# Optimization experiments

Measured on AMD Instinct MI355X. Metric: run time of the kernel, lower is better.

The kernel has to match this reference:

```python
import jax, jax.numpy as jnp
import numpy as np

DIM = 64
HEADS = 2
HD = DIM // HEADS          # 32
ALPHA = 4.0
KS = 5                     # dwc kernel size
MLP_H = 4 * DIM            # 256
LN_EPS = 1e-5


def layernorm(x, g, b):
    mu = jnp.mean(x, axis=-1, keepdims=True)
    var = jnp.mean(jnp.square(x - mu), axis=-1, keepdims=True)
    return (x - mu) * jax.lax.rsqrt(var + LN_EPS) * g + b


def safe_pow(x, p):
    # relu(x) ** p with well-defined value (and grad) at x <= 0
    xr = jnp.maximum(x, 0.0)
    safe = jnp.where(xr > 0, xr, 1.0)
    return jnp.where(xr > 0, safe ** p, 0.0)


def block_forward(x, H, W, ln1_g, ln1_b, w_qg, w_kv, pos_enc, scale_p, power_p,
                  dwc_w, dwc_b, w_proj, b_proj, ln2_g, ln2_b, w_fc1, b_fc1, w_fc2, b_fc2):
    B, N, C = x.shape
    h1 = layernorm(x, ln1_g, ln1_b)

    qg = h1 @ w_qg                         # [B,N,2C]
    q, gate = qg[..., :C], qg[..., C:]
    kv = h1 @ w_kv                         # [B,N,2C] (sr_ratio==1)
    k, v = kv[..., :C], kv[..., C:]
    k = k + pos_enc                        # [1,N,C]

    scale = jax.nn.softplus(scale_p)       # [1,1,C]
    power = 1.0 + ALPHA * jax.nn.sigmoid(power_p)  # [1,h,1,hd]
    q = q / scale
    k = k / scale

    # [B, h, N, hd]
    q = q.reshape(B, N, HEADS, HD).transpose(0, 2, 1, 3)
    k = k.reshape(B, N, HEADS, HD).transpose(0, 2, 1, 3)
    v = v.reshape(B, N, HEADS, HD).transpose(0, 2, 1, 3)

    q_pos = safe_pow(q, power)
    q_neg = safe_pow(-q, power)
    k_pos = safe_pow(k, power)
    k_neg = safe_pow(-k, power)

    q_sim = jnp.concatenate([q_pos, q_neg], axis=-1)   # [B,h,N,2hd]
    q_opp = jnp.concatenate([q_neg, q_pos], axis=-1)
    k_cat = jnp.concatenate([k_pos, k_neg], axis=-1)

    v1, v2 = v[..., :HD // 2], v[..., HD // 2:]

    n = N  # n_reduced == N for sr_ratio==1
    inv_sqrt_n = jnp.float32(n) ** -0.5
    k_mean = jnp.mean(k_cat, axis=-2)                  # [B,h,2hd]

    z_sim = 1.0 / (jnp.einsum('bhnd,bhd->bhn', q_sim, k_mean)[..., None] + 1e-6)
    kv_sim = jnp.einsum('bhnd,bhne->bhde', k_cat * inv_sqrt_n, v1 * inv_sqrt_n)
    x_sim = jnp.einsum('bhnd,bhde->bhne', q_sim, kv_sim) * z_sim

    z_opp = 1.0 / (jnp.einsum('bhnd,bhd->bhn', q_opp, k_mean)[..., None] + 1e-6)
    kv_opp = jnp.einsum('bhnd,bhne->bhde', k_cat * inv_sqrt_n, v2 * inv_sqrt_n)
    x_opp = jnp.einsum('bhnd,bhde->bhne', q_opp, kv_opp) * z_opp

    xa = jnp.concatenate([x_sim, x_opp], axis=-1)      # [B,h,N,hd]
    xa = xa.transpose(0, 2, 1, 3).reshape(B, N, C)

    # depthwise 5x5 conv over v in image layout
    v_img = v.reshape(B * HEADS, n, HD).transpose(0, 2, 1).reshape(B * HEADS, HD, H, W)
    v_dwc = jax.lax.conv_general_dilated(
        v_img, dwc_w, window_strides=(1, 1), padding='SAME',
        feature_group_count=HD, dimension_numbers=('NCHW', 'OIHW', 'NCHW'))
    v_dwc = v_dwc + dwc_b[None, :, None, None]
    v_dwc = v_dwc.reshape(B, C, H * W).transpose(0, 2, 1)  # [B,N,C]

    xa = (xa + v_dwc) * gate
    xa = xa @ w_proj + b_proj

    x = x + xa
    h2 = layernorm(x, ln2_g, ln2_b)
    m = jax.nn.gelu(h2 @ w_fc1 + b_fc1, approximate=False) @ w_fc2 + b_fc2
    return x + m


def setup_inputs() -> dict:
    key = jax.random.key(0)
    ks = jax.random.split(key, 12)
    B, H, W = 16, 128, 128
    N = H * W
    s = 0.02
    return {
        'x': jax.random.normal(ks[0], (B, N, DIM), jnp.float32),
        'H': H, 'W': W,
        'ln1_g': jnp.ones((DIM,), jnp.float32),
        'ln1_b': jnp.zeros((DIM,), jnp.float32),
        'w_qg': jax.random.normal(ks[1], (DIM, 2 * DIM), jnp.float32) * s,
        'w_kv': jax.random.normal(ks[2], (DIM, 2 * DIM), jnp.float32) * s,
        'pos_enc': jax.random.normal(ks[3], (1, N, DIM), jnp.float32) * s,
        'scale_p': jax.random.normal(ks[4], (1, 1, DIM), jnp.float32) * s,
        'power_p': jax.random.normal(ks[5], (1, HEADS, 1, HD), jnp.float32) * s,
        'dwc_w': jax.random.normal(ks[6], (HD, 1, KS, KS), jnp.float32) * s,
        'dwc_b': jnp.zeros((HD,), jnp.float32),
        'w_proj': jax.random.normal(ks[7], (DIM, DIM), jnp.float32) * s,
        'b_proj': jnp.zeros((DIM,), jnp.float32),
        'ln2_g': jnp.ones((DIM,), jnp.float32),
        'ln2_b': jnp.zeros((DIM,), jnp.float32),
        'w_fc1': jax.random.normal(ks[8], (DIM, MLP_H), jnp.float32) * s,
        'b_fc1': jnp.zeros((MLP_H,), jnp.float32),
        'w_fc2': jax.random.normal(ks[9], (MLP_H, DIM), jnp.float32) * s,
        'b_fc2': jnp.zeros((DIM,), jnp.float32),
    }


def reference(x, H, W, ln1_g, ln1_b, w_qg, w_kv, pos_enc, scale_p, power_p,
              dwc_w, dwc_b, w_proj, b_proj, ln2_g, ln2_b, w_fc1, b_fc1, w_fc2, b_fc2):
    return block_forward(x, H, W, ln1_g, ln1_b, w_qg, w_kv, pos_enc, scale_p, power_p,
                         dwc_w, dwc_b, w_proj, b_proj, ln2_g, ln2_b, w_fc1, b_fc1, w_fc2, b_fc2)
```

## Files before the change

kernel.cpp:

```cpp
#include <hip/hip_runtime.h>
#include <hip/hip_bf16.h>

#define NB 16
#define NT 16384
#define NTOK (NB * NT)

typedef __hip_bfloat16 bf16;
typedef __attribute__((ext_vector_type(8))) short short8;
typedef __attribute__((ext_vector_type(4))) float f32x4;

static __device__ __forceinline__ f32x4 MFMA(short8 a, short8 b, f32x4 c) {
    return __builtin_amdgcn_mfma_f32_16x16x32_bf16(a, b, c, 0, 0, 0);
}
static __device__ __forceinline__ short bfs(float f) {
    union { bf16 h; short s; } u; u.h = __float2bfloat16(f); return u.s;
}
static __device__ __forceinline__ float sbf(short s) {
    union { bf16 h; short s; } u; u.s = s; return __bfloat162float(u.h);
}
static __device__ __forceinline__ bf16 f2bf(float v) { return __float2bfloat16(v); }
static __device__ __forceinline__ float us2f(unsigned short u) {
    union { unsigned int i; float f; } x; x.i = ((unsigned int)u) << 16; return x.f;
}
static __device__ __forceinline__ unsigned char e8(float v) {
    union { _Float16 h; unsigned short u; } x; x.h = (_Float16)v;
    return (unsigned char)((x.u + 0x80) >> 8);
}
static __device__ __forceinline__ float d8(unsigned char e) {
    union { _Float16 h; unsigned short u; } x; x.u = (unsigned short)(e << 8);
    return (float)x.h;
}

static __device__ __forceinline__ float safe_pow(float x, float p) {
    return (x > 0.f) ? __builtin_amdgcn_exp2f(p * __builtin_amdgcn_logf(x)) : 0.f;
}
static __device__ __forceinline__ float sigm(float y) {
    return __builtin_amdgcn_rcpf(1.f + __builtin_amdgcn_exp2f(-1.44269504f * y));
}

static __device__ __forceinline__ int swb(int row, int tok) {
    return row * 64 + ((tok * 2) ^ (((row >> 1) & 3) << 4));
}

__global__ __launch_bounds__(256)
void k0_prep(const float* __restrict__ w_qg, const float* __restrict__ w_kv,
             const float* __restrict__ w_fc1, const float* __restrict__ w_fc2,
             short* __restrict__ wqk_f, short* __restrict__ wf1_f, short* __restrict__ wf2_f)
{
    int idx = blockIdx.x * 256 + threadIdx.x;
    if (idx < 16384) {
        int k = idx >> 8, col = idx & 255;
        float wv = (col < 128) ? w_qg[k * 128 + col] : w_kv[k * 128 + col - 128];
        int ct = col >> 4, ks = k >> 5, lane = (col & 15) + 16 * ((k & 31) >> 3), j = k & 7;
        wqk_f[((ct * 2 + ks) * 64 + lane) * 8 + j] = bfs(wv);
    } else if (idx < 32768) {
        int i2 = idx - 16384, k = i2 >> 8, col = i2 & 255;
        int ct = col >> 4, ks = k >> 5, lane = (col & 15) + 16 * ((k & 31) >> 3), j = k & 7;
        wf1_f[((ct * 2 + ks) * 64 + lane) * 8 + j] = bfs(w_fc1[k * 256 + col]);
    } else if (idx < 49152) {
        int i2 = idx - 32768, k = i2 >> 6, col = i2 & 63;
        int ct2 = col >> 4, ks = k >> 5, lane = (col & 15) + 16 * ((k & 31) >> 3), j = k & 7;
        wf2_f[((ct2 * 8 + ks) * 64 + lane) * 8 + j] = bfs(w_fc2[k * 64 + col]);
    }
}

__global__ __launch_bounds__(256)
void k1_proj(const float* __restrict__ x,
             const float* __restrict__ ln1_g, const float* __restrict__ ln1_b,
             const short* __restrict__ wqk_f,
             const float* __restrict__ pos_enc,
             const float* __restrict__ scale_p, const float* __restrict__ power_p,
             unsigned char* __restrict__ qb8, unsigned char* __restrict__ gbuf8,
             unsigned char* __restrict__ vbuf8,
             float* __restrict__ km_g, float* __restrict__ kv_g)
{
    __shared__ __align__(16) unsigned char lds[49152];
    __shared__ __align__(16) short wqk_s[16384];
    const int tid = threadIdx.x;
    const int b = blockIdx.y, chunk = blockIdx.x;
    const int w = tid >> 6, l = tid & 63, l15 = l & 15, g = l >> 4;
    unsigned char* kft = lds + w * 12288;
    unsigned char* vt  = kft + 8192;

    #pragma unroll
    for (int i = 0; i < 8; ++i)
        ((uint4*)wqk_s)[tid * 8 + i] = ((const uint4*)wqk_f)[tid * 8 + i];

    float g1v[16], b1v[16];
    #pragma unroll
    for (int j = 0; j < 8; j++) {
        g1v[j]     = ln1_g[g * 8 + j];      b1v[j]     = ln1_b[g * 8 + j];
        g1v[8 + j] = ln1_g[32 + g * 8 + j]; b1v[8 + j] = ln1_b[32 + g * 8 + j];
    }
    float isc[4], pwk[4];
    #pragma unroll
    for (int ct = 0; ct < 4; ct++) {
        int ch = l15 + 16 * ct;
        float s = scale_p[ch];
        float sp = 0.69314718f * __builtin_amdgcn_logf(1.f + __builtin_amdgcn_exp2f(1.44269504f * s));
        isc[ct] = __builtin_amdgcn_rcpf(sp);
        pwk[ct] = 1.f + 4.f * sigm(power_p[ch]);
    }

    f32x4 acc[2][2][4];
    #pragma unroll
    for (int s = 0; s < 2; s++)
        #pragma unroll
        for (int h = 0; h < 2; h++)
            #pragma unroll
            for (int mt = 0; mt < 4; mt++) { f32x4 z = {0.f,0.f,0.f,0.f}; acc[s][h][mt] = z; }
    float kmp[4] = {0.f,0.f,0.f,0.f}, kmn[4] = {0.f,0.f,0.f,0.f};

    __syncthreads();

    for (int it = 0; it < 8; ++it) {
        const int tok0 = chunk * 512 + (it * 4 + w) * 16;
        const size_t rowb = (size_t)b * NT + tok0;
        const float* xrow = x + (rowb + l15) * 64;
        float4 t0 = *(const float4*)(xrow + g * 8);
        float4 t1 = *(const float4*)(xrow + g * 8 + 4);
        float4 t2 = *(const float4*)(xrow + 32 + g * 8);
        float4 t3 = *(const float4*)(xrow + 32 + g * 8 + 4);
        float xa8[8] = {t0.x,t0.y,t0.z,t0.w,t1.x,t1.y,t1.z,t1.w};
        float xb8[8] = {t2.x,t2.y,t2.z,t2.w,t3.x,t3.y,t3.z,t3.w};
        float s1 = 0.f, s2 = 0.f;
        #pragma unroll
        for (int j = 0; j < 8; j++) {
            s1 += xa8[j] + xb8[j];
            s2 += xa8[j] * xa8[j] + xb8[j] * xb8[j];
        }
        s1 += __shfl_xor(s1, 16, 64); s1 += __shfl_xor(s1, 32, 64);
        s2 += __shfl_xor(s2, 16, 64); s2 += __shfl_xor(s2, 32, 64);
        float mu = s1 * 0.015625f;
        float var = s2 * 0.015625f - mu * mu;
        float rs = rsqrtf(var + 1e-5f);
        short8 A0, A1;
        #pragma unroll
        for (int j = 0; j < 8; j++) {
            A0[j] = bfs((xa8[j] - mu) * rs * g1v[j] + b1v[j]);
            A1[j] = bfs((xb8[j] - mu) * rs * g1v[8 + j] + b1v[8 + j]);
        }
        const int tokp = (it & 1) * 16;
        #pragma unroll
        for (int ct = 0; ct < 16; ct++) {
            short8 f0 = *(const short8*)(wqk_s + (ct * 2 + 0) * 512 + l * 8);
            short8 f1 = *(const short8*)(wqk_s + (ct * 2 + 1) * 512 + l * 8);
            f32x4 c = {0.f,0.f,0.f,0.f};
            c = MFMA(A0, f0, c);
            c = MFMA(A1, f1, c);
            if (ct < 4) {
                #pragma unroll
                for (int r = 0; r < 4; r++)
                    qb8[(rowb + g * 4 + r) * 64 + l15 + 16 * ct] = e8(c[r] * isc[ct]);
            } else if (ct < 8) {
                #pragma unroll
                for (int r = 0; r < 4; r++)
                    gbuf8[(rowb + g * 4 + r) * 64 + l15 + 16 * (ct - 4)] = e8(c[r]);
            } else if (ct < 12) {
                const int ctk = ct - 8, kchan = l15 + 16 * ctk;
                const int hh = kchan >> 5, d = kchan & 31;
                #pragma unroll
                for (int r = 0; r < 4; r++) {
                    int n = tok0 + g * 4 + r;
                    float kvl = (c[r] + pos_enc[(size_t)n * 64 + kchan]) * isc[ctk];
                    float kp = safe_pow(kvl, pwk[ctk]);
                    float kn = safe_pow(-kvl, pwk[ctk]);
                    kmp[ctk] += kp; kmn[ctk] += kn;
                    int tk = tokp + g * 4 + r;
                    *(short*)(kft + swb(hh * 64 + d, tk))      = bfs(kp);
                    *(short*)(kft + swb(hh * 64 + 32 + d, tk)) = bfs(kn);
                }
            } else {
                const int ctv = ct - 12, vchan = l15 + 16 * ctv;
                const int hh = vchan >> 5, vc = vchan & 31;
                #pragma unroll
                for (int r = 0; r < 4; r++) {
                    int tk = tokp + g * 4 + r;
                    vbuf8[(rowb + g * 4 + r) * 64 + vchan] = e8(c[r]);
                    *(short*)(vt + swb(hh * 32 + vc, tk)) = bfs(c[r]);
                }
            }
        }
        if (it & 1) {
            #pragma unroll
            for (int h = 0; h < 2; h++) {
                int rv0 = h * 32 + l15, rv1 = h * 32 + 16 + l15;
                short8 Bv0 = *(const short8*)(vt + rv0 * 64 + ((g * 16) ^ (((rv0 >> 1) & 3) << 4)));
                short8 Bv1 = *(const short8*)(vt + rv1 * 64 + ((g * 16) ^ (((rv1 >> 1) & 3) << 4)));
                #pragma unroll
                for (int mt = 0; mt < 4; mt++) {
                    int rk = h * 64 + mt * 16 + l15;
                    short8 Ak = *(const short8*)(kft + rk * 64 + ((g * 16) ^ (((rk >> 1) & 3) << 4)));
                    acc[0][h][mt] = MFMA(Ak, Bv0, acc[0][h][mt]);
                    acc[1][h][mt] = MFMA(Ak, Bv1, acc[1][h][mt]);
                }
            }
        }
    }
    const float invN = 1.f / 16384.f;
    float* kvb = kv_g + (size_t)b * 4096;
    #pragma unroll
    for (int s = 0; s < 2; s++)
        #pragma unroll
        for (int h = 0; h < 2; h++)
            #pragma unroll
            for (int mt = 0; mt < 4; mt++)
                #pragma unroll
                for (int r = 0; r < 4; r++)
                    atomicAdd(&kvb[((s * 2 + h) * 64 + mt * 16 + g * 4 + r) * 16 + l15],
                              acc[s][h][mt][r] * invN);
    #pragma unroll
    for (int ct = 0; ct < 4; ct++) {
        kmp[ct] += __shfl_xor(kmp[ct], 16, 64); kmp[ct] += __shfl_xor(kmp[ct], 32, 64);
        kmn[ct] += __shfl_xor(kmn[ct], 16, 64); kmn[ct] += __shfl_xor(kmn[ct], 32, 64);
    }
    if (g == 0) {
        #pragma unroll
        for (int ct = 0; ct < 4; ct++) {
            int kchan = l15 + 16 * ct, hh = kchan >> 5, d = kchan & 31;
            atomicAdd(&km_g[b * 128 + hh * 64 + d],      kmp[ct] * invN);
            atomicAdd(&km_g[b * 128 + hh * 64 + 32 + d], kmn[ct] * invN);
        }
    }
}

__global__ __launch_bounds__(256)
void k2_dwc(const unsigned char* __restrict__ vbuf8,
            const float* __restrict__ dwc_w, const float* __restrict__ dwc_b,
            unsigned char* __restrict__ vdb8)
{
    __shared__ __align__(16) unsigned short tile[12][36][64];
    const int tid = threadIdx.x;
    const int b = blockIdx.y;
    const int ty = blockIdx.x >> 2, tx = blockIdx.x & 3;
    const int y0 = ty * 8, x0 = tx * 32;

    #pragma unroll
    for (int i = 0; i < 14; ++i) {
        int cid = i * 256 + tid;
        if (cid < 3456) {
            int yy = cid / 288;
            int rem = cid - yy * 288;
            int xx = rem >> 3;
            int c8 = rem & 7;
            int Y = y0 - 2 + yy, X = x0 - 2 + xx;
            uint2 val = make_uint2(0u, 0u);
            if ((unsigned)Y < 128u && (unsigned)X < 128u)
                val = *(const uint2*)(vbuf8 + (((size_t)b * NT + Y * 128 + X) * 64 + c8 * 8));
            unsigned short ob[8];
            #pragma unroll
            for (int k = 0; k < 4; k++) {
                ob[k]     = (unsigned short)bfs(d8((unsigned char)(val.x >> (8 * k))));
                ob[4 + k] = (unsigned short)bfs(d8((unsigned char)(val.y >> (8 * k))));
            }
            uint4 o;
            o.x = (unsigned)ob[0] | ((unsigned)ob[1] << 16);
            o.y = (unsigned)ob[2] | ((unsigned)ob[3] << 16);
            o.z = (unsigned)ob[4] | ((unsigned)ob[5] << 16);
            o.w = (unsigned)ob[6] | ((unsigned)ob[7] << 16);
            *(uint4*)(&tile[yy][xx][c8 * 8]) = o;
        }
    }
    __syncthreads();

    const int w = tid >> 6, c = tid & 63, d = c & 31;
    float wt[25];
    #pragma unroll
    for (int k = 0; k < 25; k++) wt[k] = dwc_w[d * 25 + k];
    const float bias = dwc_b[d];

    #pragma unroll
    for (int yl2 = 0; yl2 < 2; ++yl2) {
        const int yl = w * 2 + yl2;
        float cw[5][5];
        #pragma unroll
        for (int xx = 0; xx < 4; ++xx)
            #pragma unroll
            for (int ky = 0; ky < 5; ++ky)
                cw[ky][xx] = us2f(tile[yl + ky][xx][c]);
        #pragma unroll
        for (int xl = 0; xl < 32; ++xl) {
            const int jn = (xl + 4) % 5;
            #pragma unroll
            for (int ky = 0; ky < 5; ++ky)
                cw[ky][jn] = us2f(tile[yl + ky][xl + 4][c]);
            float acc = bias;
            #pragma unroll
            for (int ky = 0; ky < 5; ++ky)
                #pragma unroll
                for (int kx = 0; kx < 5; ++kx)
                    acc += wt[ky * 5 + kx] * cw[ky][(xl + kx) % 5];
            const int Y = y0 + yl, X = x0 + xl;
            vdb8[((size_t)b * NT + Y * 128 + X) * 64 + c] = e8(acc);
        }
    }
}

__global__ __launch_bounds__(1024, 4)
void k3_main(const float* __restrict__ x,
             const unsigned char* __restrict__ qb8, const unsigned char* __restrict__ gbuf8,
             const unsigned char* __restrict__ vdb8,
             const float* __restrict__ km_g, const float* __restrict__ kv_g,
             const float* __restrict__ power_p,
             const float* __restrict__ w_proj, const float* __restrict__ b_proj,
             const float* __restrict__ ln2_g, const float* __restrict__ ln2_b,
             const short* __restrict__ wf1_f, const short* __restrict__ wf2_f,
             const float* __restrict__ b_fc1, const float* __restrict__ b_fc2,
             float* __restrict__ out)
{
    __shared__ __align__(16) short wkv_s[8][512];
    __shared__ __align__(16) short wp_s[8][512];
    __shared__ __align__(16) short wf1_s[16384];
    __shared__ __align__(16) short wf2_s[16384];
    __shared__ __align__(16) unsigned char tbuf[16][2048];

    const int tid = threadIdx.x, b = blockIdx.y, chunk = blockIdx.x;
    const int w = tid >> 6, l = tid & 63, l15 = l & 15, g = l >> 4;
    unsigned char* tb = tbuf[w];

    if (tid < 512) {
        int frag = tid >> 6, lane = tid & 63;
        int s2h = frag >> 1, ks = frag & 1;
        short8 v;
        #pragma unroll
        for (int j = 0; j < 8; ++j) {
            int idx = s2h * 1024 + (ks * 32 + (lane >> 4) * 8 + j) * 16 + (lane & 15);
            v[j] = bfs(kv_g[(size_t)b * 4096 + idx]);
        }
        *(short8*)&wkv_s[frag][lane * 8] = v;
    } else {
        int t2 = tid - 512;
        int frag = t2 >> 6, lane = t2 & 63;
        int ct = frag >> 1, ks = frag & 1;
        short8 v;
        #pragma unroll
        for (int j = 0; j < 8; ++j) {
            int idx = (ks * 32 + (lane >> 4) * 8 + j) * 64 + ct * 16 + (lane & 15);
            v[j] = bfs(w_proj[idx]);
        }
        *(short8*)&wp_s[frag][lane * 8] = v;
    }
    #pragma unroll
    for (int i = 0; i < 2; ++i) {
        ((uint4*)wf1_s)[tid * 2 + i] = ((const uint4*)wf1_f)[tid * 2 + i];
        ((uint4*)wf2_s)[tid * 2 + i] = ((const uint4*)wf2_f)[tid * 2 + i];
    }

    short8 Kden[2][2];
    #pragma unroll
    for (int h = 0; h < 2; ++h)
        #pragma unroll
        for (int f = 0; f < 2; ++f)
            #pragma unroll
            for (int j = 0; j < 8; ++j) {
                int d = g * 8 + j;
                float v = 0.f;
                if (l15 == 0)      v = km_g[b * 128 + h * 64 + (f ? 32 + d : d)];
                else if (l15 == 1) v = km_g[b * 128 + h * 64 + (f ? d : 32 + d)];
                Kden[h][f][j] = bfs(v);
            }

    float pw3[2][8];
    #pragma unroll
    for (int h = 0; h < 2; h++)
        #pragma unroll
        for (int j = 0; j < 8; j++)
            pw3[h][j] = 1.f + 4.f * sigm(power_p[h * 32 + g * 8 + j]);
    float bpj[4], g2[4], b2[4], bfc2v[4];
    #pragma unroll
    for (int ct = 0; ct < 4; ct++) {
        int ch = l15 + 16 * ct;
        bpj[ct] = b_proj[ch]; g2[ct] = ln2_g[ch]; b2[ct] = ln2_b[ch]; bfc2v[ct] = b_fc2[ch];
    }
    float bf1v[16];
    #pragma unroll
    for (int ct = 0; ct < 16; ct++) bf1v[ct] = b_fc1[ct * 16 + l15];

    __syncthreads();

    auto LOADIT = [&](int itx, uint2* qv, uint2* gv, uint2* vv, float (*xvv)[4]) {
        const int tok0 = chunk * 1024 + (itx * 16 + w) * 16;
        const size_t rowb = (size_t)b * NT + tok0;
        const size_t goff = (rowb + l15) * 64;
        #pragma unroll
        for (int ks = 0; ks < 2; ks++) {
            qv[ks] = *(const uint2*)(qb8   + goff + ks * 32 + g * 8);
            gv[ks] = *(const uint2*)(gbuf8 + goff + ks * 32 + g * 8);
            vv[ks] = *(const uint2*)(vdb8  + goff + ks * 32 + g * 8);
        }
        #pragma unroll
        for (int ct = 0; ct < 4; ct++)
            #pragma unroll
            for (int r = 0; r < 4; r++)
                xvv[ct][r] = x[(rowb + g * 4 + r) * 64 + l15 + 16 * ct];
    };

    uint2 qv[2], gv[2], vv[2];
    float xv[4][4];
    LOADIT(0, qv, gv, vv, xv);

    #pragma unroll
    for (int it = 0; it < 4; ++it) {
        uint2 qv2[2], gv2[2], vv2[2];
        float xv2[4][4];
        if (it < 3) LOADIT(it + 1, qv2, gv2, vv2, xv2);

        const int tok0 = chunk * 1024 + (it * 16 + w) * 16;
        const size_t rowb = (size_t)b * NT + tok0;

        float qf[2][8], vdf[2][8], ggf[2][8];
        #pragma unroll
        for (int ks = 0; ks < 2; ks++) {
            #pragma unroll
            for (int k = 0; k < 4; k++) {
                qf[ks][k]      = d8((unsigned char)(qv[ks].x >> (8 * k)));
                qf[ks][4 + k]  = d8((unsigned char)(qv[ks].y >> (8 * k)));
                ggf[ks][k]     = d8((unsigned char)(gv[ks].x >> (8 * k)));
                ggf[ks][4 + k] = d8((unsigned char)(gv[ks].y >> (8 * k)));
                vdf[ks][k]     = d8((unsigned char)(vv[ks].x >> (8 * k)));
                vdf[ks][4 + k] = d8((unsigned char)(vv[ks].y >> (8 * k)));
            }
        }

        short8 Fqp[2], Fqn[2];
        f32x4 dn[2];
        #pragma unroll
        for (int h = 0; h < 2; h++) {
            #pragma unroll
            for (int j = 0; j < 8; j++) {
                float q = qf[h][j];
                Fqp[h][j] = bfs(safe_pow(q, pw3[h][j]));
                Fqn[h][j] = bfs(safe_pow(-q, pw3[h][j]));
            }
            f32x4 z4 = {0.f, 0.f, 0.f, 0.f};
            z4 = MFMA(Fqp[h], Kden[h][0], z4);
            dn[h] = MFMA(Fqn[h], Kden[h][1], z4);
        }

        f32x4 at[4];
        #pragma unroll
        for (int hs = 0; hs < 4; hs++) { f32x4 z4 = {0.f,0.f,0.f,0.f}; at[hs] = z4; }
        #pragma unroll
        for (int h = 0; h < 2; h++) {
            short8 b00 = *(const short8*)&wkv_s[(0 * 2 + h) * 2 + 0][l * 8];
            short8 b01 = *(const short8*)&wkv_s[(0 * 2 + h) * 2 + 1][l * 8];
            short8 b10 = *(const short8*)&wkv_s[(1 * 2 + h) * 2 + 0][l * 8];
            short8 b11 = *(const short8*)&wkv_s[(1 * 2 + h) * 2 + 1][l * 8];
            at[h*2+0] = MFMA(Fqp[h], b00, at[h*2+0]);
            at[h*2+0] = MFMA(Fqn[h], b01, at[h*2+0]);
            at[h*2+1] = MFMA(Fqn[h], b10, at[h*2+1]);
            at[h*2+1] = MFMA(Fqp[h], b11, at[h*2+1]);
        }

        #pragma unroll
        for (int hs = 0; hs < 4; hs++) {
            int h = hs >> 1, s = hs & 1;
            int cb = h * 32 + s * 16;
            #pragma unroll
            for (int r = 0; r < 4; r++) {
                float dv = __shfl(dn[h][r], g * 16 + s, 64);
                float zz = __builtin_amdgcn_rcpf(dv + 1e-6f);
                int tok = g * 4 + r;
                *(short*)(tb + tok * 128 + (((cb + l15) * 2) ^ ((tok & 7) << 4))) = bfs(at[hs][r] * zz);
            }
        }
        short8 Ap[2];
        #pragma unroll
        for (int ks = 0; ks < 2; ks++) {
            short8 t8 = *(short8*)(tb + l15 * 128 + ((ks * 64 + g * 16) ^ ((l15 & 7) << 4)));
            #pragma unroll
            for (int j = 0; j < 8; j++)
                Ap[ks][j] = bfs((sbf(t8[j]) + vdf[ks][j]) * ggf[ks][j]);
        }

        f32x4 pc[4];
        #pragma unroll
        for (int ct = 0; ct < 4; ct++) {
            short8 w0 = *(const short8*)&wp_s[ct * 2 + 0][l * 8];
            short8 w1 = *(const short8*)&wp_s[ct * 2 + 1][l * 8];
            f32x4 z4 = {0.f,0.f,0.f,0.f};
            z4 = MFMA(Ap[0], w0, z4);
            pc[ct] = MFMA(Ap[1], w1, z4);
        }

        float xm[4][4];
        #pragma unroll
        for (int ct = 0; ct < 4; ct++)
            #pragma unroll
            for (int r = 0; r < 4; r++)
                xm[ct][r] = xv[ct][r] + pc[ct][r] + bpj[ct];
        #pragma unroll
        for (int r = 0; r < 4; r++) {
            float s1 = xm[0][r] + xm[1][r] + xm[2][r] + xm[3][r];
            float s2 = xm[0][r]*xm[0][r] + xm[1][r]*xm[1][r] + xm[2][r]*xm[2][r] + xm[3][r]*xm[3][r];
            #pragma unroll
            for (int m = 1; m < 16; m <<= 1) { s1 += __shfl_xor(s1, m, 64); s2 += __shfl_xor(s2, m, 64); }
            float mu = s1 * 0.015625f;
            float var = s2 * 0.015625f - mu * mu;
            float rs = rsqrtf(var + 1e-5f);
            int tok = g * 4 + r;
            #pragma unroll
            for (int ct = 0; ct < 4; ct++) {
                float h2 = (xm[ct][r] - mu) * rs * g2[ct] + b2[ct];
                *(short*)(tb + tok * 128 + (((ct * 16 + l15) * 2) ^ ((tok & 7) << 4))) = bfs(h2);
            }
        }
        short8 Ah[2];
        #pragma unroll
        for (int ks = 0; ks < 2; ks++)
            Ah[ks] = *(short8*)(tb + l15 * 128 + ((ks * 64 + g * 16) ^ ((l15 & 7) << 4)));

        f32x4 a2[4];
        #pragma unroll
        for (int ct = 0; ct < 4; ct++) { f32x4 z4 = {0.f,0.f,0.f,0.f}; a2[ct] = z4; }
        #pragma unroll
        for (int g4 = 0; g4 < 4; g4++) {
            f32x4 fc[4];
            #pragma unroll
            for (int ctl = 0; ctl < 4; ctl++) {
                int ct = g4 * 4 + ctl;
                short8 f0 = *(const short8*)(wf1_s + (ct * 2 + 0) * 512 + l * 8);
                short8 f1 = *(const short8*)(wf1_s + (ct * 2 + 1) * 512 + l * 8);
                f32x4 z4 = {0.f,0.f,0.f,0.f};
                z4 = MFMA(Ah[0], f0, z4);
                fc[ctl] = MFMA(Ah[1], f1, z4);
            }
            #pragma unroll
            for (int ctl = 0; ctl < 4; ctl++)
                #pragma unroll
                for (int r = 0; r < 4; r++) {
                    float mv = fc[ctl][r] + bf1v[g4 * 4 + ctl];
                    float gl = mv * __builtin_amdgcn_rcpf(1.f +
                        __builtin_amdgcn_exp2f(mv * (-2.30220825f - 0.10294385f * mv * mv)));
                    int tok = g * 4 + r;
                    *(short*)(tb + tok * 128 + (((ctl * 16 + l15) * 2) ^ ((tok & 7) << 4))) = bfs(gl);
                }
            #pragma unroll
            for (int ksl = 0; ksl < 2; ksl++) {
                short8 Ag = *(short8*)(tb + l15 * 128 + ((ksl * 64 + g * 16) ^ ((l15 & 7) << 4)));
                int ks = g4 * 2 + ksl;
                #pragma unroll
                for (int ct2 = 0; ct2 < 4; ct2++) {
                    short8 wv = *(const short8*)(wf2_s + (ct2 * 8 + ks) * 512 + l * 8);
                    a2[ct2] = MFMA(Ag, wv, a2[ct2]);
                }
            }
        }

        float* tb32 = (float*)tb;
        #pragma unroll
        for (int half = 0; half < 2; ++half) {
            #pragma unroll
            for (int ctl = 0; ctl < 2; ++ctl) {
                int ct = half * 2 + ctl;
                #pragma unroll
                for (int r = 0; r < 4; r++)
                    tb32[(g * 4 + r) * 32 + ctl * 16 + l15] = xm[ct][r] + a2[ct][r] + bfc2v[ct];
            }
            #pragma unroll
            for (int i = 0; i < 2; ++i) {
                f32x4 v = *(f32x4*)&tb32[i * 256 + l * 4];
                *(f32x4*)(out + (rowb + i * 8 + (l >> 3)) * 64 + half * 32 + (l & 7) * 4) = v;
            }
        }

        #pragma unroll
        for (int ks = 0; ks < 2; ks++) { qv[ks] = qv2[ks]; gv[ks] = gv2[ks]; vv[ks] = vv2[ks]; }
        #pragma unroll
        for (int ct = 0; ct < 4; ct++)
            #pragma unroll
            for (int r = 0; r < 4; r++)
                xv[ct][r] = xv2[ct][r];
    }
}

extern "C" void kernel_launch(void* const* d_in, const int* in_sizes, int n_in,
                              void* d_out, int out_size, void* d_ws, size_t ws_size,
                              hipStream_t stream)
{
    const float* x       = (const float*)d_in[0];
    const float* ln1_g   = (const float*)d_in[3];
    const float* ln1_b   = (const float*)d_in[4];
    const float* w_qg    = (const float*)d_in[5];
    const float* w_kv    = (const float*)d_in[6];
    const float* pos     = (const float*)d_in[7];
    const float* scale_p = (const float*)d_in[8];
    const float* power_p = (const float*)d_in[9];
    const float* dwc_w   = (const float*)d_in[10];
    const float* dwc_b   = (const float*)d_in[11];
    const float* w_proj  = (const float*)d_in[12];
    const float* b_proj  = (const float*)d_in[13];
    const float* ln2_g   = (const float*)d_in[14];
    const float* ln2_b   = (const float*)d_in[15];
    const float* w_fc1   = (const float*)d_in[16];
    const float* b_fc1   = (const float*)d_in[17];
    const float* w_fc2   = (const float*)d_in[18];
    const float* b_fc2   = (const float*)d_in[19];
    float* out = (float*)d_out;

    size_t ntc = (size_t)NTOK * 64;
    unsigned char* qb8   = (unsigned char*)d_ws;
    unsigned char* vbuf8 = qb8 + ntc;
    unsigned char* gbuf8 = vbuf8 + ntc;
    unsigned char* vdb8  = gbuf8 + ntc;
    float* km_g = (float*)(vdb8 + ntc);
    float* kv_g = km_g + (size_t)NB * 128;
    short* wqk_f = (short*)(kv_g + (size_t)NB * 4096);
    short* wf1_f = wqk_f + 16384;
    short* wf2_f = wf1_f + 16384;

    hipMemsetAsync(km_g, 0, ((size_t)NB * 128 + (size_t)NB * 4096) * sizeof(float), stream);

    k0_prep<<<dim3(192), 256, 0, stream>>>(w_qg, w_kv, w_fc1, w_fc2, wqk_f, wf1_f, wf2_f);
    k1_proj<<<dim3(32, NB), 256, 0, stream>>>(x, ln1_g, ln1_b, wqk_f, pos, scale_p, power_p,
                                              qb8, gbuf8, vbuf8, km_g, kv_g);
    k2_dwc<<<dim3(64, NB), 256, 0, stream>>>(vbuf8, dwc_w, dwc_b, vdb8);
    k3_main<<<dim3(16, NB), 1024, 0, stream>>>(x, qb8, gbuf8, vdb8, km_g, kv_g, power_p,
                                               w_proj, b_proj, ln2_g, ln2_b,
                                               wf1_f, wf2_f, b_fc1, b_fc2, out);
}
```

Before: 234.0 us.

## Process two 16-token tiles per wave in k1_proj and halve its grid

```diff
diff --git a/kernel.cpp b/kernel.cpp
--- a/kernel.cpp
+++ b/kernel.cpp
@@ -114,86 +114,100 @@
     __syncthreads();
 
     for (int it = 0; it < 8; ++it) {
-        const int tok0 = chunk * 512 + (it * 4 + w) * 16;
-        const size_t rowb = (size_t)b * NT + tok0;
-        const float* xrow = x + (rowb + l15) * 64;
-        float4 t0 = *(const float4*)(xrow + g * 8);
-        float4 t1 = *(const float4*)(xrow + g * 8 + 4);
-        float4 t2 = *(const float4*)(xrow + 32 + g * 8);
-        float4 t3 = *(const float4*)(xrow + 32 + g * 8 + 4);
-        float xa8[8] = {t0.x,t0.y,t0.z,t0.w,t1.x,t1.y,t1.z,t1.w};
-        float xb8[8] = {t2.x,t2.y,t2.z,t2.w,t3.x,t3.y,t3.z,t3.w};
-        float s1 = 0.f, s2 = 0.f;
-        #pragma unroll
-        for (int j = 0; j < 8; j++) {
-            s1 += xa8[j] + xb8[j];
-            s2 += xa8[j] * xa8[j] + xb8[j] * xb8[j];
-        }
-        s1 += __shfl_xor(s1, 16, 64); s1 += __shfl_xor(s1, 32, 64);
-        s2 += __shfl_xor(s2, 16, 64); s2 += __shfl_xor(s2, 32, 64);
-        float mu = s1 * 0.015625f;
-        float var = s2 * 0.015625f - mu * mu;
-        float rs = rsqrtf(var + 1e-5f);
-        short8 A0, A1;
-        #pragma unroll
-        for (int j = 0; j < 8; j++) {
-            A0[j] = bfs((xa8[j] - mu) * rs * g1v[j] + b1v[j]);
-            A1[j] = bfs((xb8[j] - mu) * rs * g1v[8 + j] + b1v[8 + j]);
-        }
-        const int tokp = (it & 1) * 16;
+        const int tokbase = chunk * 1024 + (it * 4 + w) * 32;
+        short8 A0[2], A1[2];
+        #pragma unroll
+        for (int t = 0; t < 2; ++t) {
+            const size_t rowb = (size_t)b * NT + tokbase + t * 16;
+            const float* xrow = x + (rowb + l15) * 64;
+            float4 t0 = *(const float4*)(xrow + g * 8);
+            float4 t1 = *(const float4*)(xrow + g * 8 + 4);
+            float4 t2 = *(const float4*)(xrow + 32 + g * 8);
+            float4 t3 = *(const float4*)(xrow + 32 + g * 8 + 4);
+            float xa8[8] = {t0.x,t0.y,t0.z,t0.w,t1.x,t1.y,t1.z,t1.w};
+            float xb8[8] = {t2.x,t2.y,t2.z,t2.w,t3.x,t3.y,t3.z,t3.w};
+            float s1 = 0.f, s2 = 0.f;
+            #pragma unroll
+            for (int j = 0; j < 8; j++) {
+                s1 += xa8[j] + xb8[j];
+                s2 += xa8[j] * xa8[j] + xb8[j] * xb8[j];
+            }
+            s1 += __shfl_xor(s1, 16, 64); s1 += __shfl_xor(s1, 32, 64);
+            s2 += __shfl_xor(s2, 16, 64); s2 += __shfl_xor(s2, 32, 64);
+            float mu = s1 * 0.015625f;
+            float var = s2 * 0.015625f - mu * mu;
+            float rs = rsqrtf(var + 1e-5f);
+            #pragma unroll
+            for (int j = 0; j < 8; j++) {
+                A0[t][j] = bfs((xa8[j] - mu) * rs * g1v[j] + b1v[j]);
+                A1[t][j] = bfs((xb8[j] - mu) * rs * g1v[8 + j] + b1v[8 + j]);
+            }
+        }
         #pragma unroll
         for (int ct = 0; ct < 16; ct++) {
             short8 f0 = *(const short8*)(wqk_s + (ct * 2 + 0) * 512 + l * 8);
             short8 f1 = *(const short8*)(wqk_s + (ct * 2 + 1) * 512 + l * 8);
-            f32x4 c = {0.f,0.f,0.f,0.f};
-            c = MFMA(A0, f0, c);
-            c = MFMA(A1, f1, c);
+            f32x4 c[2];
+            #pragma unroll
+            for (int t = 0; t < 2; t++) {
+                f32x4 z = {0.f,0.f,0.f,0.f};
+                z = MFMA(A0[t], f0, z);
+                c[t] = MFMA(A1[t], f1, z);
+            }
             if (ct < 4) {
                 #pragma unroll
-                for (int r = 0; r < 4; r++)
-                    qb8[(rowb + g * 4 + r) * 64 + l15 + 16 * ct] = e8(c[r] * isc[ct]);
+                for (int t = 0; t < 2; t++)
+                    #pragma unroll
+                    for (int r = 0; r < 4; r++)
+                        qb8[((size_t)b * NT + tokbase + t * 16 + g * 4 + r) * 64 + l15 + 16 * ct]
+                            = e8(c[t][r] * isc[ct]);
             } else if (ct < 8) {
                 #pragma unroll
-                for (int r = 0; r < 4; r++)
-                    gbuf8[(rowb + g * 4 + r) * 64 + l15 + 16 * (ct - 4)] = e8(c[r]);
+                for (int t = 0; t < 2; t++)
+                    #pragma unroll
+                    for (int r = 0; r < 4; r++)
+                        gbuf8[((size_t)b * NT + tokbase + t * 16 + g * 4 + r) * 64 + l15 + 16 * (ct - 4)]
+                            = e8(c[t][r]);
             } else if (ct < 12) {
                 const int ctk = ct - 8, kchan = l15 + 16 * ctk;
                 const int hh = kchan >> 5, d = kchan & 31;
                 #pragma unroll
-                for (int r = 0; r < 4; r++) {
-                    int n = tok0 + g * 4 + r;
-                    float kvl = (c[r] + pos_enc[(size_t)n * 64 + kchan]) * isc[ctk];
-                    float kp = safe_pow(kvl, pwk[ctk]);
-                    float kn = safe_pow(-kvl, pwk[ctk]);
-                    kmp[ctk] += kp; kmn[ctk] += kn;
-                    int tk = tokp + g * 4 + r;
-                    *(short*)(kft + swb(hh * 64 + d, tk))      = bfs(kp);
-                    *(short*)(kft + swb(hh * 64 + 32 + d, tk)) = bfs(kn);
-                }
+                for (int t = 0; t < 2; t++)
+                    #pragma unroll
+                    for (int r = 0; r < 4; r++) {
+                        int n = tokbase + t * 16 + g * 4 + r;
+                        float kvl = (c[t][r] + pos_enc[(size_t)n * 64 + kchan]) * isc[ctk];
+                        float kp = safe_pow(kvl, pwk[ctk]);
+                        float kn = safe_pow(-kvl, pwk[ctk]);
+                        kmp[ctk] += kp; kmn[ctk] += kn;
+                        int tk = t * 16 + g * 4 + r;
+                        *(short*)(kft + swb(hh * 64 + d, tk))      = bfs(kp);
+                        *(short*)(kft + swb(hh * 64 + 32 + d, tk)) = bfs(kn);
+                    }
             } else {
                 const int ctv = ct - 12, vchan = l15 + 16 * ctv;
                 const int hh = vchan >> 5, vc = vchan & 31;
                 #pragma unroll
-                for (int r = 0; r < 4; r++) {
-                    int tk = tokp + g * 4 + r;
-                    vbuf8[(rowb + g * 4 + r) * 64 + vchan] = e8(c[r]);
-                    *(short*)(vt + swb(hh * 32 + vc, tk)) = bfs(c[r]);
-                }
-            }
-        }
-        if (it & 1) {
-            #pragma unroll
-            for (int h = 0; h < 2; h++) {
-                int rv0 = h * 32 + l15, rv1 = h * 32 + 16 + l15;
-                short8 Bv0 = *(const short8*)(vt + rv0 * 64 + ((g * 16) ^ (((rv0 >> 1) & 3) << 4)));
-                short8 Bv1 = *(const short8*)(vt + rv1 * 64 + ((g * 16) ^ (((rv1 >> 1) & 3) << 4)));
-                #pragma unroll
-                for (int mt = 0; mt < 4; mt++) {
-                    int rk = h * 64 + mt * 16 + l15;
-                    short8 Ak = *(const short8*)(kft + rk * 64 + ((g * 16) ^ (((rk >> 1) & 3) << 4)));
-                    acc[0][h][mt] = MFMA(Ak, Bv0, acc[0][h][mt]);
-                    acc[1][h][mt] = MFMA(Ak, Bv1, acc[1][h][mt]);
-                }
+                for (int t = 0; t < 2; t++)
+                    #pragma unroll
+                    for (int r = 0; r < 4; r++) {
+                        int tk = t * 16 + g * 4 + r;
+                        vbuf8[((size_t)b * NT + tokbase + t * 16 + g * 4 + r) * 64 + vchan] = e8(c[t][r]);
+                        *(short*)(vt + swb(hh * 32 + vc, tk)) = bfs(c[t][r]);
+                    }
+            }
+        }
+        #pragma unroll
+        for (int h = 0; h < 2; h++) {
+            int rv0 = h * 32 + l15, rv1 = h * 32 + 16 + l15;
+            short8 Bv0 = *(const short8*)(vt + rv0 * 64 + ((g * 16) ^ (((rv0 >> 1) & 3) << 4)));
+            short8 Bv1 = *(const short8*)(vt + rv1 * 64 + ((g * 16) ^ (((rv1 >> 1) & 3) << 4)));
+            #pragma unroll
+            for (int mt = 0; mt < 4; mt++) {
+                int rk = h * 64 + mt * 16 + l15;
+                short8 Ak = *(const short8*)(kft + rk * 64 + ((g * 16) ^ (((rk >> 1) & 3) << 4)));
+                acc[0][h][mt] = MFMA(Ak, Bv0, acc[0][h][mt]);
+                acc[1][h][mt] = MFMA(Ak, Bv1, acc[1][h][mt]);
             }
         }
     }
@@ -612,7 +626,7 @@
     hipMemsetAsync(km_g, 0, ((size_t)NB * 128 + (size_t)NB * 4096) * sizeof(float), stream);
 
     k0_prep<<<dim3(192), 256, 0, stream>>>(w_qg, w_kv, w_fc1, w_fc2, wqk_f, wf1_f, wf2_f);
-    k1_proj<<<dim3(32, NB), 256, 0, stream>>>(x, ln1_g, ln1_b, wqk_f, pos, scale_p, power_p,
+    k1_proj<<<dim3(16, NB), 256, 0, stream>>>(x, ln1_g, ln1_b, wqk_f, pos, scale_p, power_p,
                                               qb8, gbuf8, vbuf8, km_g, kv_g);
     k2_dwc<<<dim3(64, NB), 256, 0, stream>>>(vbuf8, dwc_w, dwc_b, vdb8);
     k3_main<<<dim3(16, NB), 1024, 0, stream>>>(x, qb8, gbuf8, vdb8, km_g, kv_g, power_p,
```

New measurement: 244.5 us. 4.5% more time.
